# Kernel tuning notes

Measured on AMD Instinct MI355X. Metric: run time of the kernel, lower is better.

Reference implementation:

```python
import jax, jax.numpy as jnp
import numpy as np

B, N_PER, K = 8, 4096, 16          # graphs, nodes per graph, knn neighbors
D_IN, D_H, D_OUT = 32, 64, 128     # feature_nn: 35->64->64, global_nn: 64->128
N = B * N_PER


def setup_inputs() -> dict:
    key = jax.random.key(0)
    ks = jax.random.split(key, 8)
    sc = lambda fan: 1.0 / np.sqrt(fan)
    x = jax.random.normal(ks[0], (N, D_IN), jnp.float32)
    pos = jax.random.normal(ks[1], (N, 3), jnp.float32)
    batch = jnp.repeat(jnp.arange(B, dtype=jnp.int32), N_PER)
    fW1 = jax.random.normal(ks[2], (D_IN + 3, D_H), jnp.float32) * sc(D_IN + 3)
    fb1 = jnp.zeros((D_H,), jnp.float32)
    fW2 = jax.random.normal(ks[3], (D_H, D_H), jnp.float32) * sc(D_H)
    fb2 = jnp.zeros((D_H,), jnp.float32)
    gW = jax.random.normal(ks[4], (D_H, D_OUT), jnp.float32) * sc(D_H)
    gb = jnp.zeros((D_OUT,), jnp.float32)
    return {"x": x, "pos": pos, "batch": batch,
            "fW1": fW1, "fb1": fb1, "fW2": fW2, "fb2": fb2,
            "gW": gW, "gb": gb}


def reference(x, pos, batch, fW1, fb1, fW2, fb2, gW, gb):
    # ---- knn(pos, pos, k, batch, batch): per-graph k nearest (self included) ----
    posb = pos.reshape(B, N_PER, 3)
    sq = jnp.sum(posb * posb, axis=-1)                      # [B, Nper]
    dist = sq[:, :, None] + sq[:, None, :] - 2.0 * jnp.einsum('bnd,bmd->bnm', posb, posb)
    _, nbr = jax.lax.top_k(-dist, K)                        # [B, Nper, K] local neighbor idx
    offs = (jnp.arange(B, dtype=nbr.dtype) * N_PER)[:, None, None]
    col = (nbr + offs).reshape(-1)                          # edge_index[1]: neighbor (x) idx
    row = jnp.repeat(jnp.arange(N, dtype=col.dtype), K)     # edge_index[0]: query (y) idx

    # ---- PointConv: msg = feature_nn(cat[x_j, pos_j - pos_i]), max-aggregate at i ----
    # PyG flow source_to_target: j = edge_index[0] = row (query), i = edge_index[1] = col.
    msg = jnp.concatenate([x[row], pos[row] - pos[col]], axis=1)  # [E, 35]
    h = jax.nn.relu(msg @ fW1 + fb1)
    h = jax.nn.relu(h @ fW2 + fb2)                          # [E, 64]
    agg = jax.ops.segment_max(h, col, num_segments=N)       # max aggregation
    agg = jnp.where(jnp.isfinite(agg), agg, 0.0)            # PyG fills empty segments with 0
    out = jax.nn.relu(agg @ gW + gb)                        # global_nn
    return (out, pos, batch)
```

## Files before the change

### kernel.cpp

```cpp
#include <hip/hip_runtime.h>
#include <hip/hip_bf16.h>

#define N_PER    4096
#define KNBR     16
#define NTOT     32768
#define D_IN     32
#define D_H      64
#define D_OUT    128
#define E_TOT    (NTOT * KNBR)

#define OUT1_OFF (NTOT * D_OUT)
#define OUT2_OFF (NTOT * D_OUT + NTOT*3)

#define KNN_INF    3.4e38f
#define KNN_MARGIN 4e-3f

typedef __attribute__((ext_vector_type(8)))  short bf16x8;
typedef __attribute__((ext_vector_type(4)))  float f32x4;
typedef __attribute__((ext_vector_type(16))) float f32x16;

__device__ float          g_posf[NTOT * 3];
__device__ float          g_scf[NTOT];
__device__ __attribute__((aligned(16))) unsigned short g_knnA[NTOT * 16];
__device__ __attribute__((aligned(16))) unsigned short g_knnB[NTOT * 16];
__device__ int            g_nbr[E_TOT];
__device__ unsigned short g_base1h[NTOT * D_H];
__device__ uint4          g_Bfrag[2 * 4 * 64];
__device__ float          g_Wd[3 * D_H];
__device__ float          g_fb2v[D_H];
__device__ int            g_cnt[NTOT];
__device__ int            g_bsum[NTOT / 256];
__device__ int            g_offs[NTOT + 1];
__device__ int            g_cursor[NTOT];
__device__ int            g_inlist[E_TOT];
__device__ float          g_agg[NTOT * D_H];

__device__ __forceinline__ float ldf(const void* p, int i, int bf) {
    if (bf) return __uint_as_float(((unsigned)((const unsigned short*)p)[i]) << 16);
    return ((const float*)p)[i];
}
__device__ __forceinline__ unsigned bf16rne(float f) {
    unsigned u = __float_as_uint(f);
    return (u + 0x7FFFu + ((u >> 16) & 1u)) >> 16;
}
__device__ __forceinline__ void stf(void* p, int i, float v, int bf) {
    if (bf) ((unsigned short*)p)[i] = (unsigned short)bf16rne(v);
    else    ((float*)p)[i] = v;
}
__device__ __forceinline__ float b2f(unsigned short h) {
    return __uint_as_float(((unsigned)h) << 16);
}
__device__ __forceinline__ int wave_probe(const void* x) {
    unsigned wv = ((const unsigned*)x)[threadIdx.x & 63];
    unsigned e = (wv >> 7) & 0xFFu;
    unsigned long long mk = __ballot(e >= 110u && e <= 140u);
    return (__popcll(mk) >= 32) ? 1 : 0;
}

__global__ __launch_bounds__(256) void prep_kernel(const void* __restrict__ x,
                                                   const void* __restrict__ pos,
                                                   const void* __restrict__ fW1,
                                                   const void* __restrict__ fb1,
                                                   const void* __restrict__ fW2,
                                                   const void* __restrict__ fb2) {
    const int bf = wave_probe(x);
    const int b = blockIdx.x;
    if (b < 1024) {
        const int i0 = b * 256 + threadIdx.x;
        const int stride = 1024 * 256;
        for (int i = i0; i < NTOT * 3; i += stride) g_posf[i] = ldf(pos, i, bf);
        {
#pragma clang fp contract(off)
            for (int i = i0; i < NTOT; i += stride) {
                float a  = ldf(pos, i * 3 + 0, bf);
                float c2 = ldf(pos, i * 3 + 1, bf);
                float c3 = ldf(pos, i * 3 + 2, bf);
                float sc = a * a + c2 * c2 + c3 * c3;
                g_scf[i] = sc;
                g_cnt[i] = 0;
                unsigned hx = bf16rne(a),  hy = bf16rne(c2), hz = bf16rne(c3);
                float fhx = b2f(hx), fhy = b2f(hy), fhz = b2f(hz);
                unsigned lx = bf16rne(a - fhx), ly = bf16rne(c2 - fhy), lz = bf16rne(c3 - fhz);
                unsigned sch = bf16rne(sc);
                unsigned scl = bf16rne(sc - b2f(sch));
                unsigned nx = bf16rne(-2.0f * fhx), ny = bf16rne(-2.0f * fhy), nz = bf16rne(-2.0f * fhz);
                unsigned ox = bf16rne(-2.0f * b2f(lx)), oy = bf16rne(-2.0f * b2f(ly)), oz = bf16rne(-2.0f * b2f(lz));
                const unsigned ONEB = 0x3F80u;
                uint4 A0 = make_uint4(nx | (ny << 16), nz | (ox << 16), oy | (oz << 16), nx | (ny << 16));
                uint4 A1 = make_uint4(nz | (ONEB << 16), ONEB, 0u, 0u);
                uint4 B0 = make_uint4(hx | (hy << 16), hz | (hx << 16), hy | (hz << 16), lx | (ly << 16));
                uint4 B1 = make_uint4(lz | (sch << 16), scl, 0u, 0u);
                *(uint4*)&g_knnA[(size_t)i * 16]     = A0;
                *(uint4*)&g_knnA[(size_t)i * 16 + 8] = A1;
                *(uint4*)&g_knnB[(size_t)i * 16]     = B0;
                *(uint4*)&g_knnB[(size_t)i * 16 + 8] = B1;
            }
        }
        for (int i = i0; i < NTOT * D_H; i += stride) g_agg[i] = 0.0f;
    } else if (b < 2048) {
        int lane = threadIdx.x & 63, wid = threadIdx.x >> 6;
        int n0 = (b - 1024) * 32 + wid * 8;
        float wcol[D_IN];
#pragma unroll
        for (int k = 0; k < D_IN; k++) wcol[k] = ldf(fW1, k * D_H + lane, bf);
        float bb = ldf(fb1, lane, bf);
        if (bf) {
            const unsigned short* xp = (const unsigned short*)x;
            for (int r = 0; r < 8; r++) {
                int n = n0 + r;
                const uint4* xr = (const uint4*)(xp + (size_t)n * D_IN);
                float acc = bb;
#pragma unroll
                for (int q4 = 0; q4 < 4; q4++) {
                    uint4 w4 = xr[q4];
                    unsigned ww[4] = {w4.x, w4.y, w4.z, w4.w};
#pragma unroll
                    for (int p = 0; p < 4; p++) {
                        int k = q4 * 8 + p * 2;
                        acc += __uint_as_float(ww[p] << 16) * wcol[k];
                        acc += __uint_as_float(ww[p] & 0xFFFF0000u) * wcol[k + 1];
                    }
                }
                g_base1h[(size_t)n * D_H + lane] = (unsigned short)bf16rne(acc);
            }
        } else {
            const float* xp = (const float*)x;
            for (int r = 0; r < 8; r++) {
                int n = n0 + r;
                const float4* xr = (const float4*)(xp + (size_t)n * D_IN);
                float acc = bb;
#pragma unroll
                for (int q4 = 0; q4 < 8; q4++) {
                    float4 w4 = xr[q4];
                    int k = q4 * 4;
                    acc += w4.x * wcol[k] + w4.y * wcol[k + 1] + w4.z * wcol[k + 2] + w4.w * wcol[k + 3];
                }
                g_base1h[(size_t)n * D_H + lane] = (unsigned short)bf16rne(acc);
            }
        }
    } else {
        for (int t = threadIdx.x; t < 3 * D_H; t += 256) g_Wd[t] = ldf(fW1, D_IN * D_H + t, bf);
        if (threadIdx.x < D_H) g_fb2v[threadIdx.x] = ldf(fb2, threadIdx.x, bf);
        for (int idx = threadIdx.x; idx < 512; idx += 256) {
            int lane = idx & 63, nt = (idx >> 6) & 3, ks = idx >> 8;
            int n = nt * 16 + (lane & 15);
            int k0 = ks * 32 + ((lane >> 4) << 3);
            unsigned wds[4];
#pragma unroll
            for (int jp = 0; jp < 4; jp++) {
                unsigned lo = bf16rne(ldf(fW2, (k0 + 2 * jp) * D_H + n, bf));
                unsigned hi = bf16rne(ldf(fW2, (k0 + 2 * jp + 1) * D_H + n, bf));
                wds[jp] = lo | (hi << 16);
            }
            g_Bfrag[idx] = make_uint4(wds[0], wds[1], wds[2], wds[3]);
        }
    }
}

__device__ __forceinline__ void knn_sortval(float& v, int lane) {
#pragma unroll
    for (int k = 2; k <= 64; k <<= 1) {
#pragma unroll
        for (int j2 = k >> 1; j2 >= 1; j2 >>= 1) {
            float pv = __shfl_xor(v, j2);
            bool keepMin = (((lane & j2) == 0) == ((lane & k) == 0));
            bool tp = ((pv < v) == keepMin);
            v = tp ? pv : v;
        }
    }
}
__device__ __forceinline__ void knn_sortpair(float& d, int& idx, int lane) {
#pragma unroll
    for (int k = 2; k <= 64; k <<= 1) {
#pragma unroll
        for (int j2 = k >> 1; j2 >= 1; j2 >>= 1) {
            float pd = __shfl_xor(d, j2);
            int   pi = __shfl_xor(idx, j2);
            bool keepMin = (((lane & j2) == 0) == ((lane & k) == 0));
            bool lt = (pd < d) || (pd == d && pi < idx);
            bool tp = (lt == keepMin);
            d   = tp ? pd : d;
            idx = tp ? pi : idx;
        }
    }
}

__global__ __launch_bounds__(512) void knn_kernel() {
#pragma clang fp contract(off)
    __shared__ float          s_min[64][128];
    __shared__ float          s_T[64];
    __shared__ int            s_cnt[64];
    __shared__ unsigned short s_list[64][64];

    const int t       = threadIdx.x;
    const int lane    = t & 63;
    const int w       = t >> 6;
    const int mtile   = w & 1;
    const int quarter = w >> 1;
    const int half    = lane >> 5;
    const int col     = lane & 31;
    const int qbase   = blockIdx.x * 64;
    const int cbase   = (qbase >> 12) << 12;

    if (t < 64) s_cnt[t] = 0;

    const int qrow = qbase + mtile * 32 + col;
    const bf16x8 afrag = *(const bf16x8*)&g_knnA[(size_t)qrow * 16 + half * 8];
    const unsigned short* bp = g_knnB + (size_t)(cbase + quarter * 1024 + col) * 16 + half * 8;

    const f32x16 z = {};

    float m[16];
#pragma unroll
    for (int i = 0; i < 16; i++) m[i] = KNN_INF;
    {
        bf16x8 nb0 = *(const bf16x8*)(bp + 0 * 512);
        bf16x8 nb1 = *(const bf16x8*)(bp + 1 * 512);
        bf16x8 nb2 = *(const bf16x8*)(bp + 2 * 512);
        bf16x8 nb3 = *(const bf16x8*)(bp + 3 * 512);
        for (int g = 0; g < 8; g++) {
            bf16x8 cb0 = nb0, cb1 = nb1, cb2 = nb2, cb3 = nb3;
            if (g < 7) {
                const unsigned short* np = bp + (g + 1) * 2048;
                nb0 = *(const bf16x8*)(np + 0 * 512);
                nb1 = *(const bf16x8*)(np + 1 * 512);
                nb2 = *(const bf16x8*)(np + 2 * 512);
                nb3 = *(const bf16x8*)(np + 3 * 512);
            }
            f32x16 c0 = __builtin_amdgcn_mfma_f32_32x32x16_bf16(afrag, cb0, z, 0, 0, 0);
            f32x16 c1 = __builtin_amdgcn_mfma_f32_32x32x16_bf16(afrag, cb1, z, 0, 0, 0);
            f32x16 c2 = __builtin_amdgcn_mfma_f32_32x32x16_bf16(afrag, cb2, z, 0, 0, 0);
            f32x16 c3 = __builtin_amdgcn_mfma_f32_32x32x16_bf16(afrag, cb3, z, 0, 0, 0);
#pragma unroll
            for (int i = 0; i < 16; i++)
                m[i] = fminf(m[i], fminf(fminf(c0[i], c1[i]), fminf(c2[i], c3[i])));
        }
    }
#pragma unroll
    for (int i = 0; i < 16; i++) {
        int row = (i & 3) + 8 * (i >> 2) + 4 * half;
        s_min[mtile * 32 + row][quarter * 32 + col] = m[i];
    }
    __syncthreads();

    for (int it = 0; it < 8; it++) {
        int q = w * 8 + it;
        float v = fminf(s_min[q][lane], s_min[q][64 + lane]);
        knn_sortval(v, lane);
        if (lane == 15) s_T[q] = v + KNN_MARGIN;
    }
    __syncthreads();

    float Treg[16];
#pragma unroll
    for (int i = 0; i < 16; i++) {
        int row = (i & 3) + 8 * (i >> 2) + 4 * half;
        Treg[i] = s_T[mtile * 32 + row];
    }
    {
        bf16x8 nb0 = *(const bf16x8*)(bp + 0 * 512);
        bf16x8 nb1 = *(const bf16x8*)(bp + 1 * 512);
        bf16x8 nb2 = *(const bf16x8*)(bp + 2 * 512);
        bf16x8 nb3 = *(const bf16x8*)(bp + 3 * 512);
        for (int g = 0; g < 8; g++) {
            bf16x8 cb[4] = {nb0, nb1, nb2, nb3};
            if (g < 7) {
                const unsigned short* np = bp + (g + 1) * 2048;
                nb0 = *(const bf16x8*)(np + 0 * 512);
                nb1 = *(const bf16x8*)(np + 1 * 512);
                nb2 = *(const bf16x8*)(np + 2 * 512);
                nb3 = *(const bf16x8*)(np + 3 * 512);
            }
#pragma unroll
            for (int u = 0; u < 4; u++) {
                f32x16 c = __builtin_amdgcn_mfma_f32_32x32x16_bf16(afrag, cb[u], z, 0, 0, 0);
                int lc = quarter * 1024 + (g * 4 + u) * 32 + col;
#pragma unroll
                for (int i = 0; i < 16; i++) {
                    bool p = (c[i] <= Treg[i]);
                    unsigned long long mk = __ballot(p);
                    if (mk) {
                        int q = mtile * 32 + (i & 3) + 8 * (i >> 2) + 4 * half;
                        unsigned mk32 = (unsigned)(mk >> (half * 32));
                        int base = 0;
                        if (col == 0) base = atomicAdd(&s_cnt[q], __popc(mk32));
                        base = __shfl(base, half * 32);
                        if (p) {
                            int slot = base + __popc(mk32 & ((1u << col) - 1u));
                            if (slot < 64) s_list[q][slot] = (unsigned short)lc;
                        }
                    }
                }
            }
        }
    }
    __syncthreads();

    for (int it = 0; it < 8; it++) {
        int ql = w * 8 + it;
        int q  = qbase + ql;
        float qx = g_posf[q * 3 + 0], qy = g_posf[q * 3 + 1], qz = g_posf[q * 3 + 2];
        float qs = g_scf[q];
        int S = s_cnt[ql];
        if (S <= 64) {
            int idx = 0x7FFFFFFF;
            float d = KNN_INF;
            if (lane < S) {
                idx = cbase + (int)s_list[ql][lane];
                float px = g_posf[idx * 3], py = g_posf[idx * 3 + 1], pz = g_posf[idx * 3 + 2];
                float sc = g_scf[idx];
                float dot = px * qx + py * qy + pz * qz;
                d = (qs + sc) - 2.0f * dot;
            }
            knn_sortpair(d, idx, lane);
            if (lane < 16) {
                g_nbr[q * KNBR + lane] = idx;
                atomicAdd(&g_cnt[idx & (NTOT - 1)], 1);
            }
        } else {
            const float* cp  = g_posf + cbase * 3;
            const float* csc = g_scf + cbase;
            float lastd = -KNN_INF; int lasti = -1;
            for (int t16 = 0; t16 < 16; t16++) {
                float bd = KNN_INF; int bi = 0x7FFFFFFF;
                for (int cc = 0; cc < 64; cc++) {
                    int jj = cc * 64 + lane;
                    float px = cp[jj * 3], py = cp[jj * 3 + 1], pz = cp[jj * 3 + 2];
                    float sc = csc[jj];
                    float dot = px * qx + py * qy + pz * qz;
                    float dd = (qs + sc) - 2.0f * dot;
                    int gj = cbase + jj;
                    bool after  = (dd > lastd) || (dd == lastd && gj > lasti);
                    bool better = (dd < bd) || (dd == bd && gj < bi);
                    if (after && better) { bd = dd; bi = gj; }
                }
#pragma unroll
                for (int s2 = 1; s2 < 64; s2 <<= 1) {
                    float od = __shfl_xor(bd, s2);
                    int   oi = __shfl_xor(bi, s2);
                    if (od < bd || (od == bd && oi < bi)) { bd = od; bi = oi; }
                }
                if (lane == 0) {
                    g_nbr[q * KNBR + t16] = bi;
                    atomicAdd(&g_cnt[bi & (NTOT - 1)], 1);
                }
                lastd = bd; lasti = bi;
            }
        }
    }
}

__global__ __launch_bounds__(256) void scanA_kernel() {
    __shared__ int red[4];
    int t = threadIdx.x, lane = t & 63, w = t >> 6;
    int v = g_cnt[blockIdx.x * 256 + t];
    int s = v;
#pragma unroll
    for (int off = 1; off < 64; off <<= 1) s += __shfl_xor(s, off);
    if (lane == 0) red[w] = s;
    __syncthreads();
    if (t == 0) g_bsum[blockIdx.x] = red[0] + red[1] + red[2] + red[3];
}

__global__ __launch_bounds__(256) void scanC_kernel() {
    __shared__ int sred[4];
    __shared__ int wsum[4];
    int t = threadIdx.x, lane = t & 63, w = t >> 6;
    int contrib = (t < 128 && t < blockIdx.x) ? g_bsum[t] : 0;
    int rs = contrib;
#pragma unroll
    for (int off = 1; off < 64; off <<= 1) rs += __shfl_xor(rs, off);
    if (lane == 0) sred[w] = rs;
    __syncthreads();
    int base = sred[0] + sred[1] + sred[2] + sred[3];

    int i = blockIdx.x * 256 + t;
    int v = g_cnt[i];
    int inc = v;
#pragma unroll
    for (int off = 1; off < 64; off <<= 1) {
        int u = __shfl_up(inc, off);
        if (lane >= off) inc += u;
    }
    if (lane == 63) wsum[w] = inc;
    __syncthreads();
    int wbase = 0;
    for (int k = 0; k < w; k++) wbase += wsum[k];
    int excl = base + wbase + inc - v;
    g_offs[i] = excl;
    g_cursor[i] = excl;
    if (i == NTOT - 1) g_offs[NTOT] = E_TOT;
}

__global__ void scatter_kernel() {
    int e = blockIdx.x * 256 + threadIdx.x;
    int c = g_nbr[e] & (NTOT - 1);
    int slot = atomicAdd(&g_cursor[c], 1);
    g_inlist[slot & (E_TOT - 1)] = e;
}

__global__ __launch_bounds__(256) void edge_kernel() {
    __shared__ unsigned short sA[256 * 72];
    __shared__ int scol[256];
    const int t    = threadIdx.x;
    const int lane = t & 63;
    const int w    = t >> 6;
    const int slot0 = blockIdx.x * 256;

    {
        int e = g_inlist[slot0 + t];
        int n = (e >> 4) & (NTOT - 1);
        int j = g_nbr[e] & (NTOT - 1);
        scol[t] = j;
        float dx = g_posf[n * 3 + 0] - g_posf[j * 3 + 0];
        float dy = g_posf[n * 3 + 1] - g_posf[j * 3 + 1];
        float dz = g_posf[n * 3 + 2] - g_posf[j * 3 + 2];
        const unsigned short* b1 = g_base1h + (size_t)n * D_H;
#pragma unroll
        for (int d0 = 0; d0 < D_H; d0 += 8) {
            uint4 p = *(const uint4*)(b1 + d0);
            unsigned pw[4] = {p.x, p.y, p.z, p.w};
            unsigned qw[4];
#pragma unroll
            for (int jp = 0; jp < 4; jp++) {
                int d = d0 + 2 * jp;
                float v0 = __uint_as_float(pw[jp] << 16)
                         + dx * g_Wd[d]     + dy * g_Wd[64 + d]     + dz * g_Wd[128 + d];
                float v1 = __uint_as_float(pw[jp] & 0xFFFF0000u)
                         + dx * g_Wd[d + 1] + dy * g_Wd[64 + d + 1] + dz * g_Wd[128 + d + 1];
                v0 = fmaxf(v0, 0.f); v1 = fmaxf(v1, 0.f);
                qw[jp] = bf16rne(v0) | (bf16rne(v1) << 16);
            }
            *(uint4*)(&sA[t * 72 + d0]) = make_uint4(qw[0], qw[1], qw[2], qw[3]);
        }
    }
    __syncthreads();

    f32x4 acc[4][4];
#pragma unroll
    for (int a = 0; a < 4; a++)
#pragma unroll
        for (int b = 0; b < 4; b++) acc[a][b] = (f32x4){0.f, 0.f, 0.f, 0.f};

    const int quad = lane >> 4;
    const int l15  = lane & 15;
#pragma unroll
    for (int ks = 0; ks < 2; ks++) {
        bf16x8 bfrag[4];
#pragma unroll
        for (int nt = 0; nt < 4; nt++)
            bfrag[nt] = ((const bf16x8*)g_Bfrag)[ks * 256 + nt * 64 + lane];
#pragma unroll
        for (int mt = 0; mt < 4; mt++) {
            int row = w * 64 + mt * 16 + l15;
            bf16x8 afrag = *(const bf16x8*)(&sA[row * 72 + ks * 32 + quad * 8]);
#pragma unroll
            for (int nt = 0; nt < 4; nt++)
                acc[mt][nt] = __builtin_amdgcn_mfma_f32_16x16x32_bf16(afrag, bfrag[nt], acc[mt][nt], 0, 0, 0);
        }
    }
    __syncthreads();

#pragma unroll
    for (int nt = 0; nt < 4; nt++) {
        int dim = nt * 16 + l15;
        float bb = g_fb2v[dim];
#pragma unroll
        for (int mt = 0; mt < 4; mt++) {
#pragma unroll
            for (int r = 0; r < 4; r++) {
                int edge = w * 64 + mt * 16 + quad * 4 + r;
                float v = fmaxf(acc[mt][nt][r] + bb, 0.f);
                sA[edge * 72 + dim] = (unsigned short)bf16rne(v);
            }
        }
    }
    __syncthreads();

    {
        const int ls0 = w * 64;
        const int gs0 = slot0 + ls0;
        int cur = -1;
        float vmax = 0.f;
        for (int s = ls0; s < ls0 + 64; s++) {
            int cj = scol[s];
            float v = b2f(sA[s * 72 + lane]);
            if (cj != cur) {
                if (cur >= 0) {
                    int lo = g_offs[cur], hi = g_offs[cur + 1];
                    if (lo >= gs0 && hi <= gs0 + 64)
                        g_agg[(size_t)cur * D_H + lane] = vmax;
                    else
                        atomicMax((unsigned*)&g_agg[(size_t)cur * D_H + lane], __float_as_uint(vmax));
                }
                cur = cj; vmax = v;
            } else {
                vmax = fmaxf(vmax, v);
            }
        }
        if (cur >= 0) {
            int lo = g_offs[cur], hi = g_offs[cur + 1];
            if (lo >= gs0 && hi <= gs0 + 64)
                g_agg[(size_t)cur * D_H + lane] = vmax;
            else
                atomicMax((unsigned*)&g_agg[(size_t)cur * D_H + lane], __float_as_uint(vmax));
        }
    }
}

__global__ __launch_bounds__(256) void outmisc_kernel(const void* __restrict__ x,
                                                      const void* __restrict__ gW,
                                                      const void* __restrict__ gb,
                                                      const int* __restrict__ batch,
                                                      const void* __restrict__ pos,
                                                      void* __restrict__ out) {
    const int bf = wave_probe(x);
    const int b = blockIdx.x;
    if (b < 2048) {
        int t = threadIdx.x, d = t & 127, half = t >> 7;
        float gcol[D_H];
#pragma unroll
        for (int k = 0; k < D_H; k++) gcol[k] = ldf(gW, k * D_OUT + d, bf);
        float bb = ldf(gb, d, bf);
        int n0 = b * 16 + half * 8;
        for (int r = 0; r < 8; r++) {
            int n = n0 + r;
            float acc = bb;
#pragma unroll
            for (int k = 0; k < D_H; k++) acc += g_agg[(size_t)n * D_H + k] * gcol[k];
            stf(out, n * D_OUT + d, fmaxf(acc, 0.f), bf);
        }
    } else {
        int i = (b - 2048) * 256 + threadIdx.x;
        if (bf) {
            if (i < NTOT * 3) ((unsigned short*)out)[OUT1_OFF + i] = ((const unsigned short*)pos)[i];
            if (i < NTOT)     ((unsigned short*)out)[OUT2_OFF + i] = (unsigned short)bf16rne((float)batch[i]);
        } else {
            if (i < NTOT * 3) ((float*)out)[OUT1_OFF + i] = ((const float*)pos)[i];
            if (i < NTOT)     ((float*)out)[OUT2_OFF + i] = (float)batch[i];
        }
    }
}

extern "C" void kernel_launch(void* const* d_in, const int* in_sizes, int n_in,
                              void* d_out, int out_size, void* d_ws, size_t ws_size,
                              hipStream_t stream) {
    const void* x     = d_in[0];
    const void* pos   = d_in[1];
    const int*  batch = (const int*)d_in[2];
    const void* fW1   = d_in[3];
    const void* fb1   = d_in[4];
    const void* fW2   = d_in[5];
    const void* fb2   = d_in[6];
    const void* gW    = d_in[7];
    const void* gb    = d_in[8];

    hipLaunchKernelGGL(prep_kernel,    dim3(2049),        dim3(256), 0, stream, x, pos, fW1, fb1, fW2, fb2);
    hipLaunchKernelGGL(knn_kernel,     dim3(NTOT / 64),   dim3(512), 0, stream);
    hipLaunchKernelGGL(scanA_kernel,   dim3(NTOT / 256),  dim3(256), 0, stream);
    hipLaunchKernelGGL(scanC_kernel,   dim3(NTOT / 256),  dim3(256), 0, stream);
    hipLaunchKernelGGL(scatter_kernel, dim3(E_TOT / 256), dim3(256), 0, stream);
    hipLaunchKernelGGL(edge_kernel,    dim3(E_TOT / 256), dim3(256), 0, stream);
    hipLaunchKernelGGL(outmisc_kernel, dim3(2048 + (NTOT * 3 + 255) / 256), dim3(256), 0, stream,
                       x, gW, gb, batch, pos, d_out);
}
```

Measured before the change: 272.1 us.

## Split KNN blocks into 32 queries with 8 candidate slices per wave

The KNN kernel now handles 32 queries per block instead of 64, with each of the 8 waves scanning a 512-candidate slice rather than 2 query tiles by 4 quarters. This doubles the grid size and halves per-wave MFMA work, aiming for better occupancy and more load balance. The ballot-based compaction into the candidate list is replaced by per-lane shared atomics, which simplifies the control flow but can add LDS atomic contention when many candidates pass the threshold. Each block now reloads the full candidate set for only 32 queries, so candidate-data traffic per query doubles.

```diff
diff --git a/kernel.cpp b/kernel.cpp
--- a/kernel.cpp
+++ b/kernel.cpp
@@ -187,26 +187,24 @@
 
 __global__ __launch_bounds__(512) void knn_kernel() {
 #pragma clang fp contract(off)
-    __shared__ float          s_min[64][128];
-    __shared__ float          s_T[64];
-    __shared__ int            s_cnt[64];
-    __shared__ unsigned short s_list[64][64];
-
-    const int t       = threadIdx.x;
-    const int lane    = t & 63;
-    const int w       = t >> 6;
-    const int mtile   = w & 1;
-    const int quarter = w >> 1;
-    const int half    = lane >> 5;
-    const int col     = lane & 31;
-    const int qbase   = blockIdx.x * 64;
-    const int cbase   = (qbase >> 12) << 12;
-
-    if (t < 64) s_cnt[t] = 0;
-
-    const int qrow = qbase + mtile * 32 + col;
+    __shared__ float          s_min[32][256];
+    __shared__ float          s_T[32];
+    __shared__ int            s_cnt[32];
+    __shared__ unsigned short s_list[32][64];
+
+    const int t     = threadIdx.x;
+    const int lane  = t & 63;
+    const int w     = t >> 6;
+    const int half  = lane >> 5;
+    const int col   = lane & 31;
+    const int qbase = blockIdx.x * 32;
+    const int cbase = (qbase >> 12) << 12;
+
+    if (t < 32) s_cnt[t] = 0;
+
+    const int qrow = qbase + col;
     const bf16x8 afrag = *(const bf16x8*)&g_knnA[(size_t)qrow * 16 + half * 8];
-    const unsigned short* bp = g_knnB + (size_t)(cbase + quarter * 1024 + col) * 16 + half * 8;
+    const unsigned short* bp = g_knnB + (size_t)(cbase + w * 512 + col) * 16 + half * 8;
 
     const f32x16 z = {};
 
@@ -218,9 +216,9 @@
         bf16x8 nb1 = *(const bf16x8*)(bp + 1 * 512);
         bf16x8 nb2 = *(const bf16x8*)(bp + 2 * 512);
         bf16x8 nb3 = *(const bf16x8*)(bp + 3 * 512);
-        for (int g = 0; g < 8; g++) {
+        for (int g = 0; g < 4; g++) {
             bf16x8 cb0 = nb0, cb1 = nb1, cb2 = nb2, cb3 = nb3;
-            if (g < 7) {
+            if (g < 3) {
                 const unsigned short* np = bp + (g + 1) * 2048;
                 nb0 = *(const bf16x8*)(np + 0 * 512);
                 nb1 = *(const bf16x8*)(np + 1 * 512);
@@ -233,19 +231,20 @@
             f32x16 c3 = __builtin_amdgcn_mfma_f32_32x32x16_bf16(afrag, cb3, z, 0, 0, 0);
 #pragma unroll
             for (int i = 0; i < 16; i++)
-                m[i] = fminf(m[i], fminf(fminf(c0[i], c1[i]), fminf(c2[i], c3[i])));
+                m[i] = fminf(fminf(fminf(c0[i], c1[i]), c2[i]), fminf(c3[i], m[i]));
         }
     }
 #pragma unroll
     for (int i = 0; i < 16; i++) {
         int row = (i & 3) + 8 * (i >> 2) + 4 * half;
-        s_min[mtile * 32 + row][quarter * 32 + col] = m[i];
-    }
-    __syncthreads();
-
-    for (int it = 0; it < 8; it++) {
-        int q = w * 8 + it;
-        float v = fminf(s_min[q][lane], s_min[q][64 + lane]);
+        s_min[row][w * 32 + col] = m[i];
+    }
+    __syncthreads();
+
+    for (int it = 0; it < 4; it++) {
+        int q = w * 4 + it;
+        float v = fminf(fminf(s_min[q][lane], s_min[q][64 + lane]),
+                        fminf(s_min[q][128 + lane], s_min[q][192 + lane]));
         knn_sortval(v, lane);
         if (lane == 15) s_T[q] = v + KNN_MARGIN;
     }
@@ -255,16 +254,16 @@
 #pragma unroll
     for (int i = 0; i < 16; i++) {
         int row = (i & 3) + 8 * (i >> 2) + 4 * half;
-        Treg[i] = s_T[mtile * 32 + row];
+        Treg[i] = s_T[row];
     }
     {
         bf16x8 nb0 = *(const bf16x8*)(bp + 0 * 512);
         bf16x8 nb1 = *(const bf16x8*)(bp + 1 * 512);
         bf16x8 nb2 = *(const bf16x8*)(bp + 2 * 512);
         bf16x8 nb3 = *(const bf16x8*)(bp + 3 * 512);
-        for (int g = 0; g < 8; g++) {
+        for (int g = 0; g < 4; g++) {
             bf16x8 cb[4] = {nb0, nb1, nb2, nb3};
-            if (g < 7) {
+            if (g < 3) {
                 const unsigned short* np = bp + (g + 1) * 2048;
                 nb0 = *(const bf16x8*)(np + 0 * 512);
                 nb1 = *(const bf16x8*)(np + 1 * 512);
@@ -274,21 +273,13 @@
 #pragma unroll
             for (int u = 0; u < 4; u++) {
                 f32x16 c = __builtin_amdgcn_mfma_f32_32x32x16_bf16(afrag, cb[u], z, 0, 0, 0);
-                int lc = quarter * 1024 + (g * 4 + u) * 32 + col;
+                int lc = w * 512 + (g * 4 + u) * 32 + col;
 #pragma unroll
                 for (int i = 0; i < 16; i++) {
-                    bool p = (c[i] <= Treg[i]);
-                    unsigned long long mk = __ballot(p);
-                    if (mk) {
-                        int q = mtile * 32 + (i & 3) + 8 * (i >> 2) + 4 * half;
-                        unsigned mk32 = (unsigned)(mk >> (half * 32));
-                        int base = 0;
-                        if (col == 0) base = atomicAdd(&s_cnt[q], __popc(mk32));
-                        base = __shfl(base, half * 32);
-                        if (p) {
-                            int slot = base + __popc(mk32 & ((1u << col) - 1u));
-                            if (slot < 64) s_list[q][slot] = (unsigned short)lc;
-                        }
+                    if (c[i] <= Treg[i]) {
+                        int q = (i & 3) + 8 * (i >> 2) + 4 * half;
+                        int slot = atomicAdd(&s_cnt[q], 1);
+                        if (slot < 64) s_list[q][slot] = (unsigned short)lc;
                     }
                 }
             }
@@ -296,8 +287,8 @@
     }
     __syncthreads();
 
-    for (int it = 0; it < 8; it++) {
-        int ql = w * 8 + it;
+    for (int it = 0; it < 4; it++) {
+        int ql = w * 4 + it;
         int q  = qbase + ql;
         float qx = g_posf[q * 3 + 0], qy = g_posf[q * 3 + 1], qz = g_posf[q * 3 + 2];
         float qs = g_scf[q];
@@ -556,7 +547,7 @@
     const void* gb    = d_in[8];
 
     hipLaunchKernelGGL(prep_kernel,    dim3(2049),        dim3(256), 0, stream, x, pos, fW1, fb1, fW2, fb2);
-    hipLaunchKernelGGL(knn_kernel,     dim3(NTOT / 64),   dim3(512), 0, stream);
+    hipLaunchKernelGGL(knn_kernel,     dim3(NTOT / 32),   dim3(512), 0, stream);
     hipLaunchKernelGGL(scanA_kernel,   dim3(NTOT / 256),  dim3(256), 0, stream);
     hipLaunchKernelGGL(scanC_kernel,   dim3(NTOT / 256),  dim3(256), 0, stream);
     hipLaunchKernelGGL(scatter_kernel, dim3(E_TOT / 256), dim3(256), 0, stream);
```

After: 270.6 us. No clear change (-0.5%).
